# Performance work log

Measured on AMD Instinct MI355X. Metric: run time of the kernel, lower is better.

Reference implementation:

```python
import jax, jax.numpy as jnp
import numpy as np

EMBED_DIM = 1024
NUM_HEADS = 16
HEAD_DIM = EMBED_DIM // NUM_HEADS


def setup_inputs() -> dict:
    key = jax.random.key(0)
    k_x, k_qkv, k_proj, k_pb = jax.random.split(key, 4)
    B, N = 8, 1024
    s = 1.0 / np.sqrt(EMBED_DIM)
    return {
        "x": jax.random.normal(k_x, (B, N, EMBED_DIM), dtype=jnp.float32),
        # qkv: Linear(embed_dim -> 3*all_head_dim), bias=False
        "w_qkv": jax.random.uniform(k_qkv, (EMBED_DIM, 3 * EMBED_DIM), dtype=jnp.float32, minval=-s, maxval=s),
        # proj: Linear(all_head_dim -> embed_dim), with bias
        "w_proj": jax.random.uniform(k_proj, (EMBED_DIM, EMBED_DIM), dtype=jnp.float32, minval=-s, maxval=s),
        "b_proj": jax.random.uniform(k_pb, (EMBED_DIM,), dtype=jnp.float32, minval=-s, maxval=s),
    }


def reference(x, w_qkv, w_proj, b_proj):
    B, N, _ = x.shape
    scale = HEAD_DIM ** -0.5
    qkv = jnp.einsum("bnd,de->bne", x, w_qkv)  # [B, N, 3*D]
    q, k, v = jnp.split(qkv, 3, axis=-1)
    # reshape to heads: [B, H, N, hd]
    def heads(t):
        return t.reshape(B, N, NUM_HEADS, HEAD_DIM).transpose(0, 2, 1, 3)
    q, k, v = heads(q), heads(k), heads(v)
    attn = jnp.einsum("bhqd,bhkd->bhqk", q, k) * scale
    attn = jax.nn.softmax(attn, axis=-1)
    out = jnp.einsum("bhqk,bhkd->bhqd", attn, v)
    out = out.transpose(0, 2, 1, 3).reshape(B, N, NUM_HEADS * HEAD_DIM)
    return jnp.einsum("bnd,de->bne", out, w_proj) + b_proj
```

## Files before the change

kernel.cpp:

```cpp
#include <hip/hip_runtime.h>
#include <hip/hip_bf16.h>
#include <stdint.h>

typedef __hip_bfloat16 bf16;
typedef __attribute__((ext_vector_type(8))) __bf16 bf16x8;
typedef __attribute__((ext_vector_type(4))) float f32x4;

__device__ __forceinline__ bf16x8 load8bf(const bf16* p) {
    return __builtin_bit_cast(bf16x8, *(const int4*)p);
}

__device__ __forceinline__ void async16(const bf16* g, bf16* l) {
    __builtin_amdgcn_global_load_lds((const __attribute__((address_space(1))) void*)g,
                                     (__attribute__((address_space(3))) void*)l, 16, 0, 0);
}

__global__ __launch_bounds__(256) void cast_x_kernel(const float* __restrict__ in,
                                                     bf16* __restrict__ out, int n4) {
    int i = blockIdx.x * 256 + threadIdx.x;
    if (i >= n4) return;
    float4 v = ((const float4*)in)[i];
    ushort4 o;
    o.x = __builtin_bit_cast(unsigned short, __float2bfloat16(v.x));
    o.y = __builtin_bit_cast(unsigned short, __float2bfloat16(v.y));
    o.z = __builtin_bit_cast(unsigned short, __float2bfloat16(v.z));
    o.w = __builtin_bit_cast(unsigned short, __float2bfloat16(v.w));
    ((ushort4*)out)[i] = o;
}

__global__ __launch_bounds__(256) void transpose_cast(const float* __restrict__ in,
                                                      bf16* __restrict__ out, int R, int C) {
    __shared__ float t[32][33];
    int c0 = blockIdx.x * 32, r0 = blockIdx.y * 32;
    int tx = threadIdx.x, ty = threadIdx.y;
#pragma unroll
    for (int j = 0; j < 32; j += 8)
        t[ty + j][tx] = in[(size_t)(r0 + ty + j) * C + c0 + tx];
    __syncthreads();
#pragma unroll
    for (int j = 0; j < 32; j += 8)
        out[(size_t)(c0 + ty + j) * R + r0 + tx] = __float2bfloat16(t[tx][ty + j]);
}

template <int MODE>
__global__ __launch_bounds__(256, 4) void gemm_bt(
    const bf16* __restrict__ A, const bf16* __restrict__ Bt,
    int M, int N, int K,
    bf16* __restrict__ qo, bf16* __restrict__ ko, bf16* __restrict__ vto,
    float* __restrict__ out, const float* __restrict__ bias) {
    __shared__ __align__(16) bf16 A0[128 * 32];
    __shared__ __align__(16) bf16 B0[128 * 32];
    __shared__ __align__(16) bf16 A1[128 * 32];
    __shared__ __align__(16) bf16 B1[128 * 32];
    const int tid = threadIdx.x;
    const int l = tid & 63, wid = tid >> 6;
    const int lo = l & 15, hi = l >> 4;
    const int wm = wid >> 1, wn = wid & 1;
    const int m0 = blockIdx.x * 128, n0 = blockIdx.y * 128;
    const int tsr = tid >> 2;
    const int tsc = tid & 3;
    const int csw = (tsc ^ ((tsr >> 1) & 3)) * 8;
    const int cl  = tsc * 8;

    f32x4 acc[4][4];
#pragma unroll
    for (int i = 0; i < 4; ++i)
#pragma unroll
        for (int j = 0; j < 4; ++j) acc[i][j] = f32x4{0.f, 0.f, 0.f, 0.f};

#define STAGE32(AD, BD, KT)                                                           \
    {                                                                                 \
        async16(A + (size_t)(m0 + tsr) * K + (KT) * 32 + csw, (AD) + tsr * 32 + cl);  \
        async16(A + (size_t)(m0 + 64 + tsr) * K + (KT) * 32 + csw,                    \
                (AD) + (64 + tsr) * 32 + cl);                                         \
        async16(Bt + (size_t)(n0 + tsr) * K + (KT) * 32 + csw, (BD) + tsr * 32 + cl); \
        async16(Bt + (size_t)(n0 + 64 + tsr) * K + (KT) * 32 + csw,                   \
                (BD) + (64 + tsr) * 32 + cl);                                         \
    }

#define KB32(AC, BC, AS, BS, KT, STG)                                                 \
    {                                                                                 \
        __syncthreads();                                                              \
        if (STG) STAGE32(AS, BS, (KT) + 1)                                            \
        __builtin_amdgcn_sched_barrier(0);                                            \
        bf16x8 af[4], bf_[4];                                                         \
        _Pragma("unroll") for (int mt = 0; mt < 4; ++mt) {                            \
            int ar = wm * 64 + mt * 16 + lo;                                          \
            af[mt] = load8bf((AC) + ar * 32 + ((hi ^ ((ar >> 1) & 3)) * 8));          \
        }                                                                             \
        _Pragma("unroll") for (int nt = 0; nt < 4; ++nt) {                            \
            int br = wn * 64 + nt * 16 + lo;                                          \
            bf_[nt] = load8bf((BC) + br * 32 + ((hi ^ ((br >> 1) & 3)) * 8));         \
        }                                                                             \
        _Pragma("unroll") for (int mt = 0; mt < 4; ++mt)                              \
            _Pragma("unroll") for (int nt = 0; nt < 4; ++nt)                          \
                acc[mt][nt] = __builtin_amdgcn_mfma_f32_16x16x32_bf16(                \
                    af[mt], bf_[nt], acc[mt][nt], 0, 0, 0);                           \
    }

    const int nkt = K / 32;
    STAGE32(A0, B0, 0)
    for (int kt = 0; kt < nkt; kt += 2) {
        KB32(A0, B0, A1, B1, kt, true)
        KB32(A1, B1, A0, B0, kt + 1, (kt + 2 < nkt))
    }
#undef KB32
#undef STAGE32

#pragma unroll
    for (int mt = 0; mt < 4; ++mt)
#pragma unroll
        for (int nt = 0; nt < 4; ++nt)
#pragma unroll
            for (int r = 0; r < 4; ++r) {
                int row = m0 + wm * 64 + mt * 16 + hi * 4 + r;
                int col = n0 + wn * 64 + nt * 16 + lo;
                float v = acc[mt][nt][r];
                if (MODE == 0) {
                    if (col < 1024) {
                        qo[(size_t)row * 1024 + col] = __float2bfloat16(v * 0.125f);
                    } else if (col < 2048) {
                        ko[(size_t)row * 1024 + (col - 1024)] = __float2bfloat16(v);
                    } else {
                        int c = col - 2048;
                        vto[((size_t)(row >> 10) * 1024 + c) * 1024 + (row & 1023)] = __float2bfloat16(v);
                    }
                } else {
                    out[(size_t)row * N + col] = v + bias[col];
                }
            }
}

__global__ __launch_bounds__(256, 3) void flash_attn(
    const bf16* __restrict__ q,
    const bf16* __restrict__ kin,
    const bf16* __restrict__ vt,
    bf16* __restrict__ out)
{
    __shared__ __align__(16) bf16 Kl0[64 * 64];
    __shared__ __align__(16) bf16 Vl0[64 * 64];
    __shared__ __align__(16) bf16 Kl1[64 * 64];
    __shared__ __align__(16) bf16 Vl1[64 * 64];
    __shared__ __align__(16) bf16 Pl[4 * 32 * 72];
    const int tid = threadIdx.x;
    const int l = tid & 63, w = tid >> 6;
    const int lo = l & 15, hi = l >> 4;
    const int bid = (blockIdx.x & 7) * 128 + (blockIdx.x >> 3);
    const int qt = bid & 7, h = (bid >> 3) & 15, b = bid >> 7;
    const int ts_r = tid >> 3;
    const int ts_c = tid & 7;
    const int ts_csw = (ts_c ^ (ts_r & 7)) * 8;
    const int ts_lds = tid * 8;

    const bf16* kbase = kin + (size_t)(b * 1024) * 1024 + h * 64;
    const bf16* vbase = vt + (size_t)(b * 1024 + h * 64) * 1024;

#define STAGE_KV(KD, VD, KT)                                                          \
    {                                                                                 \
        async16(kbase + (size_t)((KT) * 64 + ts_r) * 1024 + ts_csw, (KD) + ts_lds);   \
        async16(kbase + (size_t)((KT) * 64 + 32 + ts_r) * 1024 + ts_csw,              \
                (KD) + 2048 + ts_lds);                                                \
        async16(vbase + (size_t)ts_r * 1024 + (KT) * 64 + ts_csw, (VD) + ts_lds);     \
        async16(vbase + (size_t)(32 + ts_r) * 1024 + (KT) * 64 + ts_csw,              \
                (VD) + 2048 + ts_lds);                                                \
    }

    bf16x8 qf[2][2];
#pragma unroll
    for (int mt = 0; mt < 2; ++mt)
#pragma unroll
        for (int ks = 0; ks < 2; ++ks) {
            int tok = qt * 128 + w * 32 + mt * 16 + lo;
            qf[mt][ks] = load8bf(q + (size_t)(b * 1024 + tok) * 1024 + h * 64 + ks * 32 + hi * 8);
        }

    float lsum[2][4];
    f32x4 oacc[2][4];
#pragma unroll
    for (int mt = 0; mt < 2; ++mt)
#pragma unroll
        for (int r = 0; r < 4; ++r) lsum[mt][r] = 0.f;
#pragma unroll
    for (int mt = 0; mt < 2; ++mt)
#pragma unroll
        for (int nt = 0; nt < 4; ++nt) oacc[mt][nt] = f32x4{0.f, 0.f, 0.f, 0.f};

    STAGE_KV(Kl0, Vl0, 0)
    __syncthreads();

#define FA_ITER(KC, VC, KN, VN, KT, STG)                                              \
    {                                                                                 \
        if (STG) { STAGE_KV(KN, VN, (KT) + 1) }                                       \
        __builtin_amdgcn_sched_barrier(0);                                            \
        f32x4 s[2][4];                                                                \
        _Pragma("unroll") for (int mt = 0; mt < 2; ++mt)                              \
            _Pragma("unroll") for (int nt = 0; nt < 4; ++nt)                          \
                s[mt][nt] = f32x4{0.f, 0.f, 0.f, 0.f};                                \
        _Pragma("unroll") for (int ks = 0; ks < 2; ++ks) {                            \
            bf16x8 kf[4];                                                             \
            _Pragma("unroll") for (int nt = 0; nt < 4; ++nt) {                        \
                int kr = nt * 16 + lo;                                                \
                kf[nt] = load8bf((KC) + kr * 64 + ((ks * 32 + hi * 8) ^ ((kr & 7) * 8))); \
            }                                                                         \
            _Pragma("unroll") for (int mt = 0; mt < 2; ++mt)                          \
                _Pragma("unroll") for (int nt = 0; nt < 4; ++nt)                      \
                    s[mt][nt] = __builtin_amdgcn_mfma_f32_16x16x32_bf16(              \
                        qf[mt][ks], kf[nt], s[mt][nt], 0, 0, 0);                      \
        }                                                                             \
        _Pragma("unroll") for (int mt = 0; mt < 2; ++mt)                              \
            _Pragma("unroll") for (int nt = 0; nt < 4; ++nt)                          \
                _Pragma("unroll") for (int r = 0; r < 4; ++r) {                       \
                    float p = __expf(s[mt][nt][r]);                                   \
                    lsum[mt][r] += p;                                                 \
                    Pl[(w * 32 + mt * 16 + hi * 4 + r) * 72 + nt * 16 + lo] =         \
                        __float2bfloat16(p);                                          \
                }                                                                     \
        _Pragma("unroll") for (int ks = 0; ks < 2; ++ks) {                            \
            bf16x8 vf[4], pf[2];                                                      \
            _Pragma("unroll") for (int nt = 0; nt < 4; ++nt) {                        \
                int vr = nt * 16 + lo;                                                \
                vf[nt] = load8bf((VC) + vr * 64 + ((ks * 32 + hi * 8) ^ ((vr & 7) * 8))); \
            }                                                                         \
            _Pragma("unroll") for (int mt = 0; mt < 2; ++mt)                          \
                pf[mt] = load8bf(Pl + (w * 32 + mt * 16 + lo) * 72 + ks * 32 + hi * 8); \
            _Pragma("unroll") for (int mt = 0; mt < 2; ++mt)                          \
                _Pragma("unroll") for (int nt = 0; nt < 4; ++nt)                      \
                    oacc[mt][nt] = __builtin_amdgcn_mfma_f32_16x16x32_bf16(           \
                        pf[mt], vf[nt], oacc[mt][nt], 0, 0, 0);                       \
        }                                                                             \
        __syncthreads();                                                              \
    }

    for (int kt = 0; kt < 16; kt += 2) {
        FA_ITER(Kl0, Vl0, Kl1, Vl1, kt, true)
        FA_ITER(Kl1, Vl1, Kl0, Vl0, kt + 1, (kt + 2 < 16))
    }
#undef FA_ITER
#undef STAGE_KV

#pragma unroll
    for (int mt = 0; mt < 2; ++mt)
#pragma unroll
        for (int r = 0; r < 4; ++r) {
#pragma unroll
            for (int off = 1; off < 16; off <<= 1)
                lsum[mt][r] += __shfl_xor(lsum[mt][r], off);
        }

#pragma unroll
    for (int mt = 0; mt < 2; ++mt)
#pragma unroll
        for (int nt = 0; nt < 4; ++nt)
#pragma unroll
            for (int r = 0; r < 4; ++r) {
                int tok = qt * 128 + w * 32 + mt * 16 + hi * 4 + r;
                int d = nt * 16 + lo;
                out[(size_t)(b * 1024 + tok) * 1024 + h * 64 + d] =
                    __float2bfloat16(oacc[mt][nt][r] / lsum[mt][r]);
            }
}

extern "C" void kernel_launch(void* const* d_in, const int* in_sizes, int n_in,
                              void* d_out, int out_size, void* d_ws, size_t ws_size,
                              hipStream_t stream) {
    const float* x      = (const float*)d_in[0];
    const float* w_qkv  = (const float*)d_in[1];
    const float* w_proj = (const float*)d_in[2];
    const float* b_proj = (const float*)d_in[3];
    float* out = (float*)d_out;

    char* ws = (char*)d_ws;
    bf16* xb     = (bf16*)(ws);
    bf16* wqkvT  = (bf16*)(ws + (16ull << 20));
    bf16* wprojT = (bf16*)(ws + (22ull << 20));
    bf16* qb     = (bf16*)(ws + (24ull << 20));
    bf16* kb     = (bf16*)(ws + (40ull << 20));
    bf16* vtb    = (bf16*)(ws + (56ull << 20));
    bf16* attn   = xb;

    cast_x_kernel<<<8192, 256, 0, stream>>>(x, xb, 2 * 1024 * 1024);
    transpose_cast<<<dim3(96, 32), dim3(32, 8), 0, stream>>>(w_qkv, wqkvT, 1024, 3072);
    transpose_cast<<<dim3(32, 32), dim3(32, 8), 0, stream>>>(w_proj, wprojT, 1024, 1024);
    gemm_bt<0><<<dim3(64, 24), 256, 0, stream>>>(xb, wqkvT, 8192, 3072, 1024,
                                                 qb, kb, vtb, nullptr, nullptr);
    flash_attn<<<1024, 256, 0, stream>>>(qb, kb, vtb, attn);
    gemm_bt<1><<<dim3(64, 8), 256, 0, stream>>>(attn, wprojT, 8192, 1024, 1024,
                                                nullptr, nullptr, nullptr, out, b_proj);
}
```

Measured before the change: 165.0 us.

## Enlarge GEMM tile to 256x128 with 512 threads and 64-wide K, single-buffered

The bf16 GEMM now uses 512-thread blocks computing 256x128 output tiles with a K step of 64 instead of 128x128 tiles with K step 32. It also switches from double-buffered async staging to a single LDS buffer with syncs before and after compute. The larger tile cuts global traffic per FLOP and halves loop iterations, but dropping the double buffering removes the overlap of loads with MFMA work. Fewer blocks are launched, which may hurt occupancy on a chip with many CUs.

```diff
diff --git a/kernel.cpp b/kernel.cpp
--- a/kernel.cpp
+++ b/kernel.cpp
@@ -43,23 +43,21 @@
 }
 
 template <int MODE>
-__global__ __launch_bounds__(256, 4) void gemm_bt(
+__global__ __launch_bounds__(512, 2) void gemm_bt(
     const bf16* __restrict__ A, const bf16* __restrict__ Bt,
     int M, int N, int K,
     bf16* __restrict__ qo, bf16* __restrict__ ko, bf16* __restrict__ vto,
     float* __restrict__ out, const float* __restrict__ bias) {
-    __shared__ __align__(16) bf16 A0[128 * 32];
-    __shared__ __align__(16) bf16 B0[128 * 32];
-    __shared__ __align__(16) bf16 A1[128 * 32];
-    __shared__ __align__(16) bf16 B1[128 * 32];
+    __shared__ __align__(16) bf16 Al[256 * 64];
+    __shared__ __align__(16) bf16 Bl[128 * 64];
     const int tid = threadIdx.x;
     const int l = tid & 63, wid = tid >> 6;
     const int lo = l & 15, hi = l >> 4;
-    const int wm = wid >> 1, wn = wid & 1;
-    const int m0 = blockIdx.x * 128, n0 = blockIdx.y * 128;
-    const int tsr = tid >> 2;
-    const int tsc = tid & 3;
-    const int csw = (tsc ^ ((tsr >> 1) & 3)) * 8;
+    const int wm = wid & 3, wn = wid >> 2;
+    const int m0 = blockIdx.x * 256, n0 = blockIdx.y * 128;
+    const int tsr = tid >> 3;
+    const int tsc = tid & 7;
+    const int csw = (tsc ^ (tsr & 7)) * 8;
     const int cl  = tsc * 8;
 
     f32x4 acc[4][4];
@@ -68,44 +66,46 @@
 #pragma unroll
         for (int j = 0; j < 4; ++j) acc[i][j] = f32x4{0.f, 0.f, 0.f, 0.f};
 
-#define STAGE32(AD, BD, KT)                                                           \
-    {                                                                                 \
-        async16(A + (size_t)(m0 + tsr) * K + (KT) * 32 + csw, (AD) + tsr * 32 + cl);  \
-        async16(A + (size_t)(m0 + 64 + tsr) * K + (KT) * 32 + csw,                    \
-                (AD) + (64 + tsr) * 32 + cl);                                         \
-        async16(Bt + (size_t)(n0 + tsr) * K + (KT) * 32 + csw, (BD) + tsr * 32 + cl); \
-        async16(Bt + (size_t)(n0 + 64 + tsr) * K + (KT) * 32 + csw,                   \
-                (BD) + (64 + tsr) * 32 + cl);                                         \
-    }
-
-#define KB32(AC, BC, AS, BS, KT, STG)                                                 \
-    {                                                                                 \
-        __syncthreads();                                                              \
-        if (STG) STAGE32(AS, BS, (KT) + 1)                                            \
-        __builtin_amdgcn_sched_barrier(0);                                            \
-        bf16x8 af[4], bf_[4];                                                         \
-        _Pragma("unroll") for (int mt = 0; mt < 4; ++mt) {                            \
-            int ar = wm * 64 + mt * 16 + lo;                                          \
-            af[mt] = load8bf((AC) + ar * 32 + ((hi ^ ((ar >> 1) & 3)) * 8));          \
-        }                                                                             \
-        _Pragma("unroll") for (int nt = 0; nt < 4; ++nt) {                            \
-            int br = wn * 64 + nt * 16 + lo;                                          \
-            bf_[nt] = load8bf((BC) + br * 32 + ((hi ^ ((br >> 1) & 3)) * 8));         \
-        }                                                                             \
-        _Pragma("unroll") for (int mt = 0; mt < 4; ++mt)                              \
-            _Pragma("unroll") for (int nt = 0; nt < 4; ++nt)                          \
-                acc[mt][nt] = __builtin_amdgcn_mfma_f32_16x16x32_bf16(                \
-                    af[mt], bf_[nt], acc[mt][nt], 0, 0, 0);                           \
-    }
-
-    const int nkt = K / 32;
-    STAGE32(A0, B0, 0)
-    for (int kt = 0; kt < nkt; kt += 2) {
-        KB32(A0, B0, A1, B1, kt, true)
-        KB32(A1, B1, A0, B0, kt + 1, (kt + 2 < nkt))
-    }
-#undef KB32
-#undef STAGE32
+    const int nkt = K / 64;
+    for (int kt = 0; kt < nkt; ++kt) {
+#pragma unroll
+        for (int s = 0; s < 4; ++s) {
+            int r = s * 64 + tsr;
+            async16(A + (size_t)(m0 + r) * K + kt * 64 + csw, Al + r * 64 + cl);
+        }
+#pragma unroll
+        for (int s = 0; s < 2; ++s) {
+            int r = s * 64 + tsr;
+            async16(Bt + (size_t)(n0 + r) * K + kt * 64 + csw, Bl + r * 64 + cl);
+        }
+        __syncthreads();
+        {
+            bf16x8 af[4][2], bfv[4][2];
+#pragma unroll
+            for (int mt = 0; mt < 4; ++mt) {
+                int ar = wm * 64 + mt * 16 + lo;
+#pragma unroll
+                for (int ks = 0; ks < 2; ++ks)
+                    af[mt][ks] = load8bf(Al + ar * 64 + ((ks * 32 + hi * 8) ^ ((ar & 7) * 8)));
+            }
+#pragma unroll
+            for (int nt = 0; nt < 4; ++nt) {
+                int br = wn * 64 + nt * 16 + lo;
+#pragma unroll
+                for (int ks = 0; ks < 2; ++ks)
+                    bfv[nt][ks] = load8bf(Bl + br * 64 + ((ks * 32 + hi * 8) ^ ((br & 7) * 8)));
+            }
+#pragma unroll
+            for (int mt = 0; mt < 4; ++mt)
+#pragma unroll
+                for (int nt = 0; nt < 4; ++nt)
+#pragma unroll
+                    for (int ks = 0; ks < 2; ++ks)
+                        acc[mt][nt] = __builtin_amdgcn_mfma_f32_16x16x32_bf16(
+                            af[mt][ks], bfv[nt][ks], acc[mt][nt], 0, 0, 0);
+        }
+        __syncthreads();
+    }
 
 #pragma unroll
     for (int mt = 0; mt < 4; ++mt)
@@ -281,9 +281,9 @@
     cast_x_kernel<<<8192, 256, 0, stream>>>(x, xb, 2 * 1024 * 1024);
     transpose_cast<<<dim3(96, 32), dim3(32, 8), 0, stream>>>(w_qkv, wqkvT, 1024, 3072);
     transpose_cast<<<dim3(32, 32), dim3(32, 8), 0, stream>>>(w_proj, wprojT, 1024, 1024);
-    gemm_bt<0><<<dim3(64, 24), 256, 0, stream>>>(xb, wqkvT, 8192, 3072, 1024,
+    gemm_bt<0><<<dim3(32, 24), 512, 0, stream>>>(xb, wqkvT, 8192, 3072, 1024,
                                                  qb, kb, vtb, nullptr, nullptr);
     flash_attn<<<1024, 256, 0, stream>>>(qb, kb, vtb, attn);
-    gemm_bt<1><<<dim3(64, 8), 256, 0, stream>>>(attn, wprojT, 8192, 1024, 1024,
+    gemm_bt<1><<<dim3(32, 8), 512, 0, stream>>>(attn, wprojT, 8192, 1024, 1024,
                                                 nullptr, nullptr, nullptr, out, b_proj);
 }
```

Measured after the change: 162.3 us. No clear change (-1.6%).

## Enlarge GEMM tiles to 256x256 with BK=64 and split-phase async staging

Applied to the files above, without the earlier changes.

Both bf16 GEMMs now use 256x256 output tiles with a K-step of 64 and 512 threads per block, each wave holding a 128x64 accumulator. A and B are staged into LDS at different points in the iteration: the next B tile is issued before the MFMAs, and the A tile two steps ahead is issued after a mid-iteration barrier, separated by explicit vmcnt/lgkmcnt waits. An XOR swizzle is used for the 64-wide rows, and s_setprio is raised around the MFMA sections. The aim is more data reuse per global load and better overlap of loads with compute. In exchange the K loop is hardcoded to 1024, LDS use per block rises to about 128KB, and far fewer blocks are launched (128 for the projection GEMM), which can leave CUs idle.

```diff
diff --git a/kernel.cpp b/kernel.cpp
--- a/kernel.cpp
+++ b/kernel.cpp
@@ -43,77 +43,116 @@
 }
 
 template <int MODE>
-__global__ __launch_bounds__(256, 4) void gemm_bt(
+__global__ __launch_bounds__(512, 2) void gemm_bt(
     const bf16* __restrict__ A, const bf16* __restrict__ Bt,
     int M, int N, int K,
     bf16* __restrict__ qo, bf16* __restrict__ ko, bf16* __restrict__ vto,
     float* __restrict__ out, const float* __restrict__ bias) {
-    __shared__ __align__(16) bf16 A0[128 * 32];
-    __shared__ __align__(16) bf16 B0[128 * 32];
-    __shared__ __align__(16) bf16 A1[128 * 32];
-    __shared__ __align__(16) bf16 B1[128 * 32];
+    __shared__ __align__(16) bf16 A0[256 * 64];
+    __shared__ __align__(16) bf16 B0[256 * 64];
+    __shared__ __align__(16) bf16 A1[256 * 64];
+    __shared__ __align__(16) bf16 B1[256 * 64];
     const int tid = threadIdx.x;
     const int l = tid & 63, wid = tid >> 6;
     const int lo = l & 15, hi = l >> 4;
-    const int wm = wid >> 1, wn = wid & 1;
-    const int m0 = blockIdx.x * 128, n0 = blockIdx.y * 128;
-    const int tsr = tid >> 2;
-    const int tsc = tid & 3;
-    const int csw = (tsc ^ ((tsr >> 1) & 3)) * 8;
-    const int cl  = tsc * 8;
-
-    f32x4 acc[4][4];
-#pragma unroll
-    for (int i = 0; i < 4; ++i)
+    const int wm = wid & 1, wn = wid >> 1;
+    const int m0 = blockIdx.x * 256, n0 = blockIdx.y * 256;
+
+    f32x4 acc[8][4];
+#pragma unroll
+    for (int i = 0; i < 8; ++i)
 #pragma unroll
         for (int j = 0; j < 4; ++j) acc[i][j] = f32x4{0.f, 0.f, 0.f, 0.f};
 
-#define STAGE32(AD, BD, KT)                                                           \
+#define STAGE_FULL(SRC, BASE, DST, KT)                                                \
+    _Pragma("unroll") for (int s_ = 0; s_ < 4; ++s_) {                                \
+        int r_ = s_ * 64 + (tid >> 3);                                                \
+        int c_ = tid & 7;                                                             \
+        async16((SRC) + (size_t)((BASE) + r_) * K + (KT) * 64 + ((c_ ^ (r_ & 7)) * 8),\
+                (DST) + s_ * 4096 + tid * 8);                                         \
+    }
+
+#define TILE256(AC, BC, BO, KT, STG1, STG2, ENDW)                                     \
     {                                                                                 \
-        async16(A + (size_t)(m0 + tsr) * K + (KT) * 32 + csw, (AD) + tsr * 32 + cl);  \
-        async16(A + (size_t)(m0 + 64 + tsr) * K + (KT) * 32 + csw,                    \
-                (AD) + (64 + tsr) * 32 + cl);                                         \
-        async16(Bt + (size_t)(n0 + tsr) * K + (KT) * 32 + csw, (BD) + tsr * 32 + cl); \
-        async16(Bt + (size_t)(n0 + 64 + tsr) * K + (KT) * 32 + csw,                   \
-                (BD) + (64 + tsr) * 32 + cl);                                         \
-    }
-
-#define KB32(AC, BC, AS, BS, KT, STG)                                                 \
-    {                                                                                 \
-        __syncthreads();                                                              \
-        if (STG) STAGE32(AS, BS, (KT) + 1)                                            \
-        __builtin_amdgcn_sched_barrier(0);                                            \
-        bf16x8 af[4], bf_[4];                                                         \
-        _Pragma("unroll") for (int mt = 0; mt < 4; ++mt) {                            \
-            int ar = wm * 64 + mt * 16 + lo;                                          \
-            af[mt] = load8bf((AC) + ar * 32 + ((hi ^ ((ar >> 1) & 3)) * 8));          \
+        if (STG1) { STAGE_FULL(Bt, n0, BO, (KT) + 1) }                                \
+        __builtin_amdgcn_sched_barrier(0);                                            \
+        bf16x8 a_[8][2], b_[4][2];                                                    \
+        _Pragma("unroll") for (int mt = 0; mt < 8; ++mt) {                            \
+            int ar = wm * 128 + mt * 16 + lo;                                         \
+            _Pragma("unroll") for (int ks = 0; ks < 2; ++ks)                          \
+                a_[mt][ks] = load8bf((AC) + ar * 64 +                                 \
+                                     ((ks * 32 + hi * 8) ^ ((ar & 7) * 8)));          \
         }                                                                             \
         _Pragma("unroll") for (int nt = 0; nt < 4; ++nt) {                            \
             int br = wn * 64 + nt * 16 + lo;                                          \
-            bf_[nt] = load8bf((BC) + br * 32 + ((hi ^ ((br >> 1) & 3)) * 8));         \
+            _Pragma("unroll") for (int ks = 0; ks < 2; ++ks)                          \
+                b_[nt][ks] = load8bf((BC) + br * 64 +                                 \
+                                     ((ks * 32 + hi * 8) ^ ((br & 7) * 8)));          \
         }                                                                             \
+        __builtin_amdgcn_s_setprio(1);                                                \
         _Pragma("unroll") for (int mt = 0; mt < 4; ++mt)                              \
             _Pragma("unroll") for (int nt = 0; nt < 4; ++nt)                          \
-                acc[mt][nt] = __builtin_amdgcn_mfma_f32_16x16x32_bf16(                \
-                    af[mt], bf_[nt], acc[mt][nt], 0, 0, 0);                           \
-    }
-
-    const int nkt = K / 32;
-    STAGE32(A0, B0, 0)
-    for (int kt = 0; kt < nkt; kt += 2) {
-        KB32(A0, B0, A1, B1, kt, true)
-        KB32(A1, B1, A0, B0, kt + 1, (kt + 2 < nkt))
-    }
-#undef KB32
-#undef STAGE32
-
-#pragma unroll
-    for (int mt = 0; mt < 4; ++mt)
+                _Pragma("unroll") for (int ks = 0; ks < 2; ++ks)                      \
+                    acc[mt][nt] = __builtin_amdgcn_mfma_f32_16x16x32_bf16(            \
+                        a_[mt][ks], b_[nt][ks], acc[mt][nt], 0, 0, 0);                \
+        __builtin_amdgcn_s_setprio(0);                                                \
+        asm volatile("s_waitcnt lgkmcnt(0)" ::: "memory");                            \
+        __builtin_amdgcn_sched_barrier(0);                                            \
+        __builtin_amdgcn_s_barrier();             \
+        __builtin_amdgcn_sched_barrier(0);                                            \
+        if (STG2) { STAGE_FULL(A, m0, AC, (KT) + 2) }                                 \
+        __builtin_amdgcn_sched_barrier(0);                                            \
+        __builtin_amdgcn_s_setprio(1);                                                \
+        _Pragma("unroll") for (int mt = 4; mt < 8; ++mt)                              \
+            _Pragma("unroll") for (int nt = 0; nt < 4; ++nt)                          \
+                _Pragma("unroll") for (int ks = 0; ks < 2; ++ks)                      \
+                    acc[mt][nt] = __builtin_amdgcn_mfma_f32_16x16x32_bf16(            \
+                        a_[mt][ks], b_[nt][ks], acc[mt][nt], 0, 0, 0);                \
+        __builtin_amdgcn_s_setprio(0);                                                \
+        __builtin_amdgcn_sched_barrier(0);                                            \
+        ENDW                                                                          \
+    }
+
+#define ENDW4                                                                         \
+    asm volatile("s_waitcnt vmcnt(4)" ::: "memory");                                  \
+    __builtin_amdgcn_sched_barrier(0);                                                \
+    __builtin_amdgcn_s_barrier();                                                     \
+    __builtin_amdgcn_sched_barrier(0);
+#define ENDW0                                                                         \
+    asm volatile("s_waitcnt vmcnt(0)" ::: "memory");                                  \
+    __builtin_amdgcn_sched_barrier(0);                                                \
+    __builtin_amdgcn_s_barrier();                                                     \
+    __builtin_amdgcn_sched_barrier(0);
+#define ENDWN
+
+    STAGE_FULL(A, m0, A0, 0)
+    STAGE_FULL(Bt, n0, B0, 0)
+    STAGE_FULL(A, m0, A1, 1)
+    __builtin_amdgcn_sched_barrier(0);
+    asm volatile("s_waitcnt vmcnt(4)" ::: "memory");
+    __builtin_amdgcn_sched_barrier(0);
+    __builtin_amdgcn_s_barrier();
+    __builtin_amdgcn_sched_barrier(0);
+
+    for (int kt = 0; kt < 14; kt += 2) {
+        TILE256(A0, B0, B1, kt, 1, 1, ENDW4)
+        TILE256(A1, B1, B0, kt + 1, 1, 1, ENDW4)
+    }
+    TILE256(A0, B0, B1, 14, 1, 0, ENDW0)
+    TILE256(A1, B1, B0, 15, 0, 0, ENDWN)
+#undef ENDWN
+#undef ENDW0
+#undef ENDW4
+#undef TILE256
+#undef STAGE_FULL
+
+#pragma unroll
+    for (int mt = 0; mt < 8; ++mt)
 #pragma unroll
         for (int nt = 0; nt < 4; ++nt)
 #pragma unroll
             for (int r = 0; r < 4; ++r) {
-                int row = m0 + wm * 64 + mt * 16 + hi * 4 + r;
+                int row = m0 + wm * 128 + mt * 16 + hi * 4 + r;
                 int col = n0 + wn * 64 + nt * 16 + lo;
                 float v = acc[mt][nt][r];
                 if (MODE == 0) {
@@ -281,9 +320,9 @@
     cast_x_kernel<<<8192, 256, 0, stream>>>(x, xb, 2 * 1024 * 1024);
     transpose_cast<<<dim3(96, 32), dim3(32, 8), 0, stream>>>(w_qkv, wqkvT, 1024, 3072);
     transpose_cast<<<dim3(32, 32), dim3(32, 8), 0, stream>>>(w_proj, wprojT, 1024, 1024);
-    gemm_bt<0><<<dim3(64, 24), 256, 0, stream>>>(xb, wqkvT, 8192, 3072, 1024,
+    gemm_bt<0><<<dim3(32, 12), 512, 0, stream>>>(xb, wqkvT, 8192, 3072, 1024,
                                                  qb, kb, vtb, nullptr, nullptr);
     flash_attn<<<1024, 256, 0, stream>>>(qb, kb, vtb, attn);
-    gemm_bt<1><<<dim3(64, 8), 256, 0, stream>>>(attn, wprojT, 8192, 1024, 1024,
+    gemm_bt<1><<<dim3(32, 4), 512, 0, stream>>>(attn, wprojT, 8192, 1024, 1024,
                                                 nullptr, nullptr, nullptr, out, b_proj);
 }
```

Measured after the change: 231.5 us. 1.4x slower.
